# Kernel tuning notes

Measured on AMD Instinct MI355X. Metric: run time of the kernel, lower is better.

Reference implementation:

```python
import jax, jax.numpy as jnp
import numpy as np

B, N_N, N_A, D = 1024, 96, 96, 512


def _normalize(x):
    return x / jnp.linalg.norm(x, axis=-1, keepdims=True)


def setup_inputs() -> dict:
    key = jax.random.key(0)
    ks = jax.random.split(key, 8)
    img_embs = _normalize(jax.random.normal(ks[0], (B, D), jnp.float32))
    normal_text_embs = _normalize(jax.random.normal(ks[1], (N_N, D), jnp.float32))
    abnormal_text_embs = _normalize(jax.random.normal(ks[2], (N_A, D), jnp.float32))
    logit_scale = jnp.full((1,), np.log(100.0), jnp.float32)  # CLIP temperature
    W1 = jax.random.normal(ks[3], (2 * D, D), jnp.float32) / np.sqrt(2 * D)
    b1 = jnp.zeros((D,), jnp.float32)
    W2 = jax.random.normal(ks[4], (D, D // 2), jnp.float32) / np.sqrt(D)
    b2 = jnp.zeros((D // 2,), jnp.float32)
    W3 = jax.random.normal(ks[5], (D // 2, D // 4), jnp.float32) / np.sqrt(D // 2)
    b3 = jnp.zeros((D // 4,), jnp.float32)
    return {"img_embs": img_embs, "normal_text_embs": normal_text_embs,
            "abnormal_text_embs": abnormal_text_embs, "logit_scale": logit_scale,
            "W1": W1, "b1": b1, "W2": W2, "b2": b2, "W3": W3, "b3": b3}


def _mlp(x, W1, b1, W2, b2, W3, b3):
    h = jax.nn.relu(x @ W1 + b1)
    h = jax.nn.relu(h @ W2 + b2)
    return h @ W3 + b3


def _branch(img_embs, text_embs, scale, W1, b1, W2, b2, W3, b3):
    # sims: [B, N]; softmax weights then exp-scaled text embeddings
    sims = (img_embs @ text_embs.T) * scale
    w = jax.nn.softmax(sims, axis=-1)
    scaled_text = text_embs[None, :, :] * jnp.exp(w)[:, :, None]      # [B, N, D]
    rep_img = jnp.broadcast_to(img_embs[:, None, :], scaled_text.shape)  # [B, N, D]
    x = jnp.concatenate([rep_img, scaled_text], axis=-1)              # [B, N, 2D]
    h = _mlp(x, W1, b1, W2, b2, W3, b3)                               # [B, N, D//4]
    return h.mean(axis=1)                                             # [B, D//4]


def reference(img_embs, normal_text_embs, abnormal_text_embs, logit_scale,
              W1, b1, W2, b2, W3, b3):
    scale = jnp.exp(logit_scale[0])
    h_n = _branch(img_embs, normal_text_embs, scale, W1, b1, W2, b2, W3, b3)
    h_a = _branch(img_embs, abnormal_text_embs, scale, W1, b1, W2, b2, W3, b3)
    return (h_n, h_a)
```

## Files before the change

kernel.cpp:

```cpp
#include <hip/hip_runtime.h>
#include <hip/hip_bf16.h>


typedef __attribute__((ext_vector_type(8))) short short8;
typedef __attribute__((ext_vector_type(4))) float floatx4;
typedef __attribute__((ext_vector_type(4))) unsigned int uint4v;

__device__ __forceinline__ unsigned short f2bf(float x) {
    unsigned int u = __float_as_uint(x);
    u += 0x7fffu + ((u >> 16) & 1u);
    return (unsigned short)(u >> 16);
}
__device__ __forceinline__ float bf2f(unsigned short u) {
    return __uint_as_float(((unsigned int)u) << 16);
}

template <bool BF16OUT>
__device__ __forceinline__ void gemm64(
    const float* __restrict__ A0, const float* __restrict__ A1, int rows0,
    const float* __restrict__ Bm, float* __restrict__ Cf,
    unsigned short* __restrict__ Cb, int bx, int by,
    unsigned char* smem, int t) {
    float (*sAT)[68] = (float (*)[68])smem;
    int r0b = bx * 64, c0b = by * 64;
    int rg = t >> 4, cg = t & 15;
    int c0 = c0b + cg * 4;
    float acc[4][4];
#pragma unroll
    for (int r = 0; r < 4; r++)
#pragma unroll
        for (int c = 0; c < 4; c++) acc[r][c] = 0.f;

    for (int k0 = 0; k0 < 512; k0 += 32) {
#pragma unroll
        for (int i = 0; i < 2; i++) {
            int row = (t >> 3) + i * 32;
            int kk = (t & 7) * 4;
            int gr = r0b + row;
            const float* Ap = (gr < rows0) ? (A0 + gr * 512) : (A1 + (gr - rows0) * 512);
            float4 av = *(const float4*)(Ap + k0 + kk);
            sAT[kk + 0][row] = av.x; sAT[kk + 1][row] = av.y;
            sAT[kk + 2][row] = av.z; sAT[kk + 3][row] = av.w;
        }
        __syncthreads();
#pragma unroll
        for (int kk = 0; kk < 32; kk++) {
            float4 a = *(const float4*)(&sAT[kk][rg * 4]);
            float4 bv = *(const float4*)(Bm + (k0 + kk) * 512 + c0);
            float ar[4] = {a.x, a.y, a.z, a.w};
            float bc[4] = {bv.x, bv.y, bv.z, bv.w};
#pragma unroll
            for (int r = 0; r < 4; r++)
#pragma unroll
                for (int c = 0; c < 4; c++)
                    acc[r][c] = fmaf(ar[r], bc[c], acc[r][c]);
        }
        __syncthreads();
    }
    int r0 = r0b + rg * 4;
#pragma unroll
    for (int r = 0; r < 4; r++) {
        if (BF16OUT) {
            unsigned long long pk =
                (unsigned long long)f2bf(acc[r][0]) |
                ((unsigned long long)f2bf(acc[r][1]) << 16) |
                ((unsigned long long)f2bf(acc[r][2]) << 32) |
                ((unsigned long long)f2bf(acc[r][3]) << 48);
            *(unsigned long long*)(Cb + (r0 + r) * 512 + c0) = pk;
        } else {
            *(float4*)(Cf + (r0 + r) * 512 + c0) =
                make_float4(acc[r][0], acc[r][1], acc[r][2], acc[r][3]);
        }
    }
}

__global__ __launch_bounds__(256) void prep_kernel(
    const float* __restrict__ img, const float* __restrict__ tn,
    const float* __restrict__ ta, const float* __restrict__ ls,
    const float* __restrict__ W1, const float* __restrict__ W2,
    float* __restrict__ e_ws, float* __restrict__ U_ws,
    unsigned short* __restrict__ Tb, unsigned short* __restrict__ W2T) {
    __shared__ __align__(16) unsigned char smem[9216];
    int idx = blockIdx.x;
    int t = threadIdx.x;

    if (idx < 1024) {
        int b = idx;
        float* sImg = (float*)smem;
        float* sS   = sImg + 512;
        float* sMx  = sS + 192;
        float* sSum = sMx + 2;
        for (int i = t; i < 512; i += 256) sImg[i] = img[b * 512 + i];
        __syncthreads();
        float scale = __expf(ls[0]);
        int g = t & 7;
#pragma unroll
        for (int i = 0; i < 6; i++) {
            int n = (t >> 3) + 32 * i;
            const float* tx = (n < 96) ? (tn + n * 512) : (ta + (n - 96) * 512);
            float d = 0.f;
#pragma unroll
            for (int s = 0; s < 16; s++) {
                int k = g * 4 + s * 32;
                float4 x = *(const float4*)(tx + k);
                d += x.x * sImg[k] + x.y * sImg[k + 1] + x.z * sImg[k + 2] + x.w * sImg[k + 3];
            }
            d += __shfl_xor(d, 1);
            d += __shfl_xor(d, 2);
            d += __shfl_xor(d, 4);
            if (g == 0) sS[n] = d * scale;
        }
        __syncthreads();
        if (t < 2) {
            float m = -1e30f;
            for (int n = 0; n < 96; n++) m = fmaxf(m, sS[t * 96 + n]);
            float s = 0.f;
            for (int n = 0; n < 96; n++) s += __expf(sS[t * 96 + n] - m);
            sMx[t] = m; sSum[t] = s;
        }
        __syncthreads();
        if (t < 192) {
            int br = t / 96, n = t % 96;
            float w = __expf(sS[t] - sMx[br]) / sSum[br];
            e_ws[(br * 1024 + b) * 96 + n] = __expf(w);
        }
    } else if (idx < 1152) {
        int i = idx - 1024;
        gemm64<false>(img, img, 1 << 20, W1, U_ws, nullptr, i & 15, i >> 4, smem, t);
    } else if (idx < 1176) {
        int i = idx - 1152;
        gemm64<true>(tn, ta, 96, W1 + 512 * 512, nullptr, Tb, i % 3, i / 3, smem, t);
    } else {
        int i = idx - 1176;
        int n0 = i * 64;
        for (int r = 0; r < 64; r++) {
            int n = n0 + r;
            for (int k = t; k < 512; k += 256)
                W2T[n * 512 + k] = f2bf(W2[k * 256 + n]);
        }
    }
}

__global__ __launch_bounds__(256) void branch_mlp2(
    const float* __restrict__ U, const unsigned short* __restrict__ Tb,
    const float* __restrict__ e_all, const unsigned short* __restrict__ W2T,
    const float* __restrict__ b1, const float* __restrict__ b2,
    const float* __restrict__ W3, const float* __restrict__ b3,
    float* __restrict__ out) {
    int b = blockIdx.x, br = blockIdx.y;
    const unsigned short* T = Tb + br * (96 * 512);
    const float* e = e_all + (br * 1024 + b) * 96;

    __shared__ float sUb[512];
    __shared__ float sE[96];
    __shared__ __align__(16) unsigned short sH[96][88];
    __shared__ float sM2[256];
    __shared__ float sPart[256];

    int t = threadIdx.x;
    for (int i = t; i < 512; i += 256) sUb[i] = U[b * 512 + i] + b1[i];
    if (t < 96) sE[t] = e[t];
    __syncthreads();

    const int wave = t >> 6, lane = t & 63;
    const int frow = lane & 15, fkq = (lane >> 4) * 8;
    const int ncol0 = wave * 64;
    const int srow = t >> 3;
    const int skc = (t & 7) * 8;

    const floatx4 fz = {0.f, 0.f, 0.f, 0.f};
    floatx4 acc[6][4];
#pragma unroll
    for (int mt = 0; mt < 6; mt++)
#pragma unroll
        for (int j = 0; j < 4; j++) acc[mt][j] = fz;

    int trow[3]; float ev[3]; short8 tv[3];
#pragma unroll
    for (int i2 = 0; i2 < 3; i2++) {
        trow[i2] = srow + 32 * i2;
        ev[i2] = sE[trow[i2]];
        tv[i2] = *(const short8*)(T + trow[i2] * 512 + skc);
    }

#pragma unroll
    for (int kt = 0; kt < 8; kt++) {
        int k0 = kt * 64;
        float4 u0 = *(const float4*)(&sUb[k0 + skc]);
        float4 u1 = *(const float4*)(&sUb[k0 + skc + 4]);
        float ua[8] = {u0.x, u0.y, u0.z, u0.w, u1.x, u1.y, u1.z, u1.w};
#pragma unroll
        for (int i2 = 0; i2 < 3; i2++) {
            uint4v pk;
#pragma unroll
            for (int jj = 0; jj < 4; jj++) {
                float f0 = fmaxf(fmaf(ev[i2], bf2f((unsigned short)tv[i2][2 * jj]), ua[2 * jj]), 0.f);
                float f1 = fmaxf(fmaf(ev[i2], bf2f((unsigned short)tv[i2][2 * jj + 1]), ua[2 * jj + 1]), 0.f);
                __hip_bfloat162 h2 = __float22bfloat162_rn(make_float2(f0, f1));
                unsigned int bits;
                __builtin_memcpy(&bits, &h2, 4);
                pk[jj] = bits;
            }
            *(uint4v*)(&sH[trow[i2]][skc]) = pk;
        }
        __syncthreads();
        if (kt < 7) {
#pragma unroll
            for (int i2 = 0; i2 < 3; i2++)
                tv[i2] = *(const short8*)(T + trow[i2] * 512 + k0 + 64 + skc);
        }
#pragma unroll
        for (int ks = 0; ks < 2; ks++) {
            short8 bfr[4];
#pragma unroll
            for (int j = 0; j < 4; j++)
                bfr[j] = *(const short8*)(W2T + (ncol0 + j * 16 + frow) * 512 + k0 + ks * 32 + fkq);
#pragma unroll
            for (int mt = 0; mt < 6; mt++) {
                short8 afr = *(const short8*)(&sH[mt * 16 + frow][ks * 32 + fkq]);
#pragma unroll
                for (int j = 0; j < 4; j++)
                    acc[mt][j] = __builtin_amdgcn_mfma_f32_16x16x32_bf16(afr, bfr[j], acc[mt][j], 0, 0, 0);
            }
        }
        __syncthreads();
    }

#pragma unroll
    for (int j = 0; j < 4; j++) {
        int col = ncol0 + j * 16 + frow;
        float bb = b2[col];
        float s = 0.f;
#pragma unroll
        for (int mt = 0; mt < 6; mt++)
#pragma unroll
            for (int r = 0; r < 4; r++)
                s += fmaxf(acc[mt][j][r] + bb, 0.f);
        s += __shfl_xor(s, 16);
        s += __shfl_xor(s, 32);
        if (lane < 16) sM2[col] = s * (1.0f / 96.0f);
    }
    __syncthreads();

    int col = t & 127, ks2 = t >> 7;
    const float* w3p = W3 + (ks2 * 128) * 128 + col;
    const float* mp = sM2 + ks2 * 128;
    float o = 0.f;
#pragma unroll 8
    for (int k = 0; k < 128; k++) o = fmaf(mp[k], w3p[k * 128], o);
    sPart[t] = o;
    __syncthreads();
    if (t < 128) out[(br * 1024 + b) * 128 + t] = sPart[t] + sPart[t + 128] + b3[t];
}

extern "C" void kernel_launch(void* const* d_in, const int* in_sizes, int n_in,
                              void* d_out, int out_size, void* d_ws, size_t ws_size,
                              hipStream_t stream) {
    const float* img = (const float*)d_in[0];
    const float* tn  = (const float*)d_in[1];
    const float* ta  = (const float*)d_in[2];
    const float* ls  = (const float*)d_in[3];
    const float* W1  = (const float*)d_in[4];
    const float* b1  = (const float*)d_in[5];
    const float* W2  = (const float*)d_in[6];
    const float* b2  = (const float*)d_in[7];
    const float* W3  = (const float*)d_in[8];
    const float* b3  = (const float*)d_in[9];
    float* out = (float*)d_out;
    float* ws  = (float*)d_ws;

    float* e_ws = ws;
    float* U_ws = ws + 196608;
    unsigned short* Tb  = (unsigned short*)(ws + 720896);
    unsigned short* W2T = (unsigned short*)(ws + 770048);

    prep_kernel<<<1180, 256, 0, stream>>>(img, tn, ta, ls, W1, W2, e_ws, U_ws, Tb, W2T);
    branch_mlp2<<<dim3(1024, 2), 256, 0, stream>>>(U_ws, Tb, e_ws, W2T, b1, b2, W3, b3, out);
}
```

Before: 214.7 us.

## Build MFMA A-fragments in registers and use finer prep GEMM tiles

The branch MLP kernel no longer stages the relu'd layer-1 activations through shared memory with block barriers. Each wave now loads T rows straight from global memory in MFMA fragment layout and forms the bf16 A operand in registers. This removes the LDS round trip and the __syncthreads per k-tile. The cost is that every wave recomputes the same activation fragments (4x redundant elementwise work and T loads). Separately, the prep GEMMs switch from 64x64 register-blocked tiles to 16x64 tiles with one row per thread, giving many more blocks but less data reuse per block.

```diff
diff --git a/kernel.cpp b/kernel.cpp
--- a/kernel.cpp
+++ b/kernel.cpp
@@ -4,7 +4,6 @@
 
 typedef __attribute__((ext_vector_type(8))) short short8;
 typedef __attribute__((ext_vector_type(4))) float floatx4;
-typedef __attribute__((ext_vector_type(4))) unsigned int uint4v;
 
 __device__ __forceinline__ unsigned short f2bf(float x) {
     unsigned int u = __float_as_uint(x);
@@ -16,61 +15,38 @@
 }
 
 template <bool BF16OUT>
-__device__ __forceinline__ void gemm64(
+__device__ __forceinline__ void gemm16(
     const float* __restrict__ A0, const float* __restrict__ A1, int rows0,
     const float* __restrict__ Bm, float* __restrict__ Cf,
-    unsigned short* __restrict__ Cb, int bx, int by,
-    unsigned char* smem, int t) {
-    float (*sAT)[68] = (float (*)[68])smem;
-    int r0b = bx * 64, c0b = by * 64;
-    int rg = t >> 4, cg = t & 15;
-    int c0 = c0b + cg * 4;
-    float acc[4][4];
-#pragma unroll
-    for (int r = 0; r < 4; r++)
-#pragma unroll
-        for (int c = 0; c < 4; c++) acc[r][c] = 0.f;
-
+    unsigned short* __restrict__ Cb, int mt, int nt, float* sA , int t) {
+    int r0 = mt * 16, c0 = nt * 64;
+    int row = t >> 4, cg = t & 15;
+    int rglob = r0 + row;
+    const float* Ap = (rglob < rows0) ? (A0 + rglob * 512) : (A1 + (rglob - rows0) * 512);
+    float a0 = 0.f, a1 = 0.f, a2 = 0.f, a3 = 0.f;
+    const float* Bp = Bm + c0 + cg * 4;
     for (int k0 = 0; k0 < 512; k0 += 32) {
-#pragma unroll
-        for (int i = 0; i < 2; i++) {
-            int row = (t >> 3) + i * 32;
-            int kk = (t & 7) * 4;
-            int gr = r0b + row;
-            const float* Ap = (gr < rows0) ? (A0 + gr * 512) : (A1 + (gr - rows0) * 512);
-            float4 av = *(const float4*)(Ap + k0 + kk);
-            sAT[kk + 0][row] = av.x; sAT[kk + 1][row] = av.y;
-            sAT[kk + 2][row] = av.z; sAT[kk + 3][row] = av.w;
-        }
-        __syncthreads();
-#pragma unroll
+        __syncthreads();
+        float2 av = *(const float2*)(Ap + k0 + cg * 2);
+        sA[row * 33 + cg * 2] = av.x;
+        sA[row * 33 + cg * 2 + 1] = av.y;
+        __syncthreads();
+#pragma unroll 8
         for (int kk = 0; kk < 32; kk++) {
-            float4 a = *(const float4*)(&sAT[kk][rg * 4]);
-            float4 bv = *(const float4*)(Bm + (k0 + kk) * 512 + c0);
-            float ar[4] = {a.x, a.y, a.z, a.w};
-            float bc[4] = {bv.x, bv.y, bv.z, bv.w};
-#pragma unroll
-            for (int r = 0; r < 4; r++)
-#pragma unroll
-                for (int c = 0; c < 4; c++)
-                    acc[r][c] = fmaf(ar[r], bc[c], acc[r][c]);
-        }
-        __syncthreads();
-    }
-    int r0 = r0b + rg * 4;
-#pragma unroll
-    for (int r = 0; r < 4; r++) {
-        if (BF16OUT) {
-            unsigned long long pk =
-                (unsigned long long)f2bf(acc[r][0]) |
-                ((unsigned long long)f2bf(acc[r][1]) << 16) |
-                ((unsigned long long)f2bf(acc[r][2]) << 32) |
-                ((unsigned long long)f2bf(acc[r][3]) << 48);
-            *(unsigned long long*)(Cb + (r0 + r) * 512 + c0) = pk;
-        } else {
-            *(float4*)(Cf + (r0 + r) * 512 + c0) =
-                make_float4(acc[r][0], acc[r][1], acc[r][2], acc[r][3]);
-        }
+            float a = sA[row * 33 + kk];
+            float4 bv = *(const float4*)(Bp + (k0 + kk) * 512);
+            a0 = fmaf(a, bv.x, a0); a1 = fmaf(a, bv.y, a1);
+            a2 = fmaf(a, bv.z, a2); a3 = fmaf(a, bv.w, a3);
+        }
+    }
+    int c = c0 + cg * 4;
+    if (BF16OUT) {
+        unsigned long long pk =
+            (unsigned long long)f2bf(a0) | ((unsigned long long)f2bf(a1) << 16) |
+            ((unsigned long long)f2bf(a2) << 32) | ((unsigned long long)f2bf(a3) << 48);
+        *(unsigned long long*)(Cb + rglob * 512 + c) = pk;
+    } else {
+        *(float4*)(Cf + rglob * 512 + c) = make_float4(a0, a1, a2, a3);
     }
 }
 
@@ -80,16 +56,16 @@
     const float* __restrict__ W1, const float* __restrict__ W2,
     float* __restrict__ e_ws, float* __restrict__ U_ws,
     unsigned short* __restrict__ Tb, unsigned short* __restrict__ W2T) {
-    __shared__ __align__(16) unsigned char smem[9216];
+    __shared__ __align__(16) float smem[720];
     int idx = blockIdx.x;
     int t = threadIdx.x;
 
     if (idx < 1024) {
         int b = idx;
-        float* sImg = (float*)smem;
-        float* sS   = sImg + 512;
-        float* sMx  = sS + 192;
-        float* sSum = sMx + 2;
+        float* sImg = smem;
+        float* sS   = smem + 512;
+        float* sMx  = smem + 704;
+        float* sSum = smem + 706;
         for (int i = t; i < 512; i += 256) sImg[i] = img[b * 512 + i];
         __syncthreads();
         float scale = __expf(ls[0]);
@@ -124,24 +100,23 @@
             float w = __expf(sS[t] - sMx[br]) / sSum[br];
             e_ws[(br * 1024 + b) * 96 + n] = __expf(w);
         }
-    } else if (idx < 1152) {
+    } else if (idx < 1536) {
         int i = idx - 1024;
-        gemm64<false>(img, img, 1 << 20, W1, U_ws, nullptr, i & 15, i >> 4, smem, t);
-    } else if (idx < 1176) {
-        int i = idx - 1152;
-        gemm64<true>(tn, ta, 96, W1 + 512 * 512, nullptr, Tb, i % 3, i / 3, smem, t);
+        gemm16<false>(img, img, 1 << 20, W1, U_ws, nullptr, i >> 3, i & 7, smem, t);
+    } else if (idx < 1632) {
+        int i = idx - 1536;
+        gemm16<true>(tn, ta, 96, W1 + 512 * 512, nullptr, Tb, i >> 3, i & 7, smem, t);
     } else {
-        int i = idx - 1176;
-        int n0 = i * 64;
-        for (int r = 0; r < 64; r++) {
-            int n = n0 + r;
+        int i = idx - 1632;
+        for (int r = 0; r < 16; r++) {
+            int n = i * 16 + r;
             for (int k = t; k < 512; k += 256)
                 W2T[n * 512 + k] = f2bf(W2[k * 256 + n]);
         }
     }
 }
 
-__global__ __launch_bounds__(256) void branch_mlp2(
+__global__ __launch_bounds__(256) void branch_mlp3(
     const float* __restrict__ U, const unsigned short* __restrict__ Tb,
     const float* __restrict__ e_all, const unsigned short* __restrict__ W2T,
     const float* __restrict__ b1, const float* __restrict__ b2,
@@ -149,24 +124,24 @@
     float* __restrict__ out) {
     int b = blockIdx.x, br = blockIdx.y;
     const unsigned short* T = Tb + br * (96 * 512);
-    const float* e = e_all + (br * 1024 + b) * 96;
 
     __shared__ float sUb[512];
     __shared__ float sE[96];
-    __shared__ __align__(16) unsigned short sH[96][88];
     __shared__ float sM2[256];
     __shared__ float sPart[256];
 
     int t = threadIdx.x;
     for (int i = t; i < 512; i += 256) sUb[i] = U[b * 512 + i] + b1[i];
-    if (t < 96) sE[t] = e[t];
+    if (t < 96) sE[t] = e_all[(br * 1024 + b) * 96 + t];
     __syncthreads();
 
     const int wave = t >> 6, lane = t & 63;
     const int frow = lane & 15, fkq = (lane >> 4) * 8;
     const int ncol0 = wave * 64;
-    const int srow = t >> 3;
-    const int skc = (t & 7) * 8;
+
+    float ev[6];
+#pragma unroll
+    for (int mt = 0; mt < 6; mt++) ev[mt] = sE[mt * 16 + frow];
 
     const floatx4 fz = {0.f, 0.f, 0.f, 0.f};
     floatx4 acc[6][4];
@@ -175,55 +150,36 @@
 #pragma unroll
         for (int j = 0; j < 4; j++) acc[mt][j] = fz;
 
-    int trow[3]; float ev[3]; short8 tv[3];
-#pragma unroll
-    for (int i2 = 0; i2 < 3; i2++) {
-        trow[i2] = srow + 32 * i2;
-        ev[i2] = sE[trow[i2]];
-        tv[i2] = *(const short8*)(T + trow[i2] * 512 + skc);
-    }
-
-#pragma unroll
-    for (int kt = 0; kt < 8; kt++) {
-        int k0 = kt * 64;
-        float4 u0 = *(const float4*)(&sUb[k0 + skc]);
-        float4 u1 = *(const float4*)(&sUb[k0 + skc + 4]);
+    const unsigned short* Trow = T + frow * 512 + fkq;
+    const unsigned short* Brow = W2T + (ncol0 + frow) * 512 + fkq;
+
+#pragma unroll 2
+    for (int s = 0; s < 16; s++) {
+        int k0 = s * 32;
+        float4 u0 = *(const float4*)(&sUb[k0 + fkq]);
+        float4 u1 = *(const float4*)(&sUb[k0 + fkq + 4]);
         float ua[8] = {u0.x, u0.y, u0.z, u0.w, u1.x, u1.y, u1.z, u1.w};
-#pragma unroll
-        for (int i2 = 0; i2 < 3; i2++) {
-            uint4v pk;
+        short8 bfr[4];
+#pragma unroll
+        for (int j = 0; j < 4; j++)
+            bfr[j] = *(const short8*)(Brow + j * (16 * 512) + k0);
+#pragma unroll
+        for (int mt = 0; mt < 6; mt++) {
+            short8 tv = *(const short8*)(Trow + mt * (16 * 512) + k0);
+            short8 afr;
 #pragma unroll
             for (int jj = 0; jj < 4; jj++) {
-                float f0 = fmaxf(fmaf(ev[i2], bf2f((unsigned short)tv[i2][2 * jj]), ua[2 * jj]), 0.f);
-                float f1 = fmaxf(fmaf(ev[i2], bf2f((unsigned short)tv[i2][2 * jj + 1]), ua[2 * jj + 1]), 0.f);
+                float f0 = fmaxf(fmaf(ev[mt], bf2f((unsigned short)tv[2 * jj]), ua[2 * jj]), 0.f);
+                float f1 = fmaxf(fmaf(ev[mt], bf2f((unsigned short)tv[2 * jj + 1]), ua[2 * jj + 1]), 0.f);
                 __hip_bfloat162 h2 = __float22bfloat162_rn(make_float2(f0, f1));
                 unsigned int bits;
                 __builtin_memcpy(&bits, &h2, 4);
-                pk[jj] = bits;
+                ((unsigned int*)&afr)[jj] = bits;
             }
-            *(uint4v*)(&sH[trow[i2]][skc]) = pk;
-        }
-        __syncthreads();
-        if (kt < 7) {
-#pragma unroll
-            for (int i2 = 0; i2 < 3; i2++)
-                tv[i2] = *(const short8*)(T + trow[i2] * 512 + k0 + 64 + skc);
-        }
-#pragma unroll
-        for (int ks = 0; ks < 2; ks++) {
-            short8 bfr[4];
 #pragma unroll
             for (int j = 0; j < 4; j++)
-                bfr[j] = *(const short8*)(W2T + (ncol0 + j * 16 + frow) * 512 + k0 + ks * 32 + fkq);
-#pragma unroll
-            for (int mt = 0; mt < 6; mt++) {
-                short8 afr = *(const short8*)(&sH[mt * 16 + frow][ks * 32 + fkq]);
-#pragma unroll
-                for (int j = 0; j < 4; j++)
-                    acc[mt][j] = __builtin_amdgcn_mfma_f32_16x16x32_bf16(afr, bfr[j], acc[mt][j], 0, 0, 0);
-            }
-        }
-        __syncthreads();
+                acc[mt][j] = __builtin_amdgcn_mfma_f32_16x16x32_bf16(afr, bfr[j], acc[mt][j], 0, 0, 0);
+        }
     }
 
 #pragma unroll
@@ -274,6 +230,6 @@
     unsigned short* Tb  = (unsigned short*)(ws + 720896);
     unsigned short* W2T = (unsigned short*)(ws + 770048);
 
-    prep_kernel<<<1180, 256, 0, stream>>>(img, tn, ta, ls, W1, W2, e_ws, U_ws, Tb, W2T);
-    branch_mlp2<<<dim3(1024, 2), 256, 0, stream>>>(U_ws, Tb, e_ws, W2T, b1, b2, W3, b3, out);
-}
+    prep_kernel<<<1648, 256, 0, stream>>>(img, tn, ta, ls, W1, W2, e_ws, U_ws, Tb, W2T);
+    branch_mlp3<<<dim3(1024, 2), 256, 0, stream>>>(U_ws, Tb, e_ws, W2T, b1, b2, W3, b3, out);
+}
```

New measurement: 325.3 us. 1.52x slower.

## Double-buffer hidden tile in LDS and prefetch W2 fragments across k-steps

Applied to the files above, without the earlier changes.

The hidden-activation LDS tile becomes double-buffered, which removes the second barrier per k-iteration. W2T fragments for the next k-step are prefetched into registers before the barrier so global load latency overlaps with compute. Launch bounds now request two blocks per CU. The trade-off is extra register and LDS pressure, and the tighter launch bound could force register spills.

```diff
diff --git a/kernel.cpp b/kernel.cpp
--- a/kernel.cpp
+++ b/kernel.cpp
@@ -141,7 +141,7 @@
     }
 }
 
-__global__ __launch_bounds__(256) void branch_mlp2(
+__global__ __launch_bounds__(256, 2) void branch_mlp4(
     const float* __restrict__ U, const unsigned short* __restrict__ Tb,
     const float* __restrict__ e_all, const unsigned short* __restrict__ W2T,
     const float* __restrict__ b1, const float* __restrict__ b2,
@@ -149,17 +149,16 @@
     float* __restrict__ out) {
     int b = blockIdx.x, br = blockIdx.y;
     const unsigned short* T = Tb + br * (96 * 512);
-    const float* e = e_all + (br * 1024 + b) * 96;
 
     __shared__ float sUb[512];
     __shared__ float sE[96];
-    __shared__ __align__(16) unsigned short sH[96][88];
+    __shared__ __align__(16) unsigned short sH[2][96][88];
     __shared__ float sM2[256];
     __shared__ float sPart[256];
 
     int t = threadIdx.x;
     for (int i = t; i < 512; i += 256) sUb[i] = U[b * 512 + i] + b1[i];
-    if (t < 96) sE[t] = e[t];
+    if (t < 96) sE[t] = e_all[(br * 1024 + b) * 96 + t];
     __syncthreads();
 
     const int wave = t >> 6, lane = t & 63;
@@ -182,10 +181,15 @@
         ev[i2] = sE[trow[i2]];
         tv[i2] = *(const short8*)(T + trow[i2] * 512 + skc);
     }
-
-#pragma unroll
-    for (int kt = 0; kt < 8; kt++) {
-        int k0 = kt * 64;
+    const unsigned short* Bbase = W2T + (ncol0 + frow) * 512 + fkq;
+    short8 bpre[4];
+#pragma unroll
+    for (int j = 0; j < 4; j++)
+        bpre[j] = *(const short8*)(Bbase + j * (16 * 512));
+
+#pragma unroll
+    for (int s = 0; s < 8; s++) {
+        int k0 = s * 64;
         float4 u0 = *(const float4*)(&sUb[k0 + skc]);
         float4 u1 = *(const float4*)(&sUb[k0 + skc + 4]);
         float ua[8] = {u0.x, u0.y, u0.z, u0.w, u1.x, u1.y, u1.z, u1.w};
@@ -201,29 +205,38 @@
                 __builtin_memcpy(&bits, &h2, 4);
                 pk[jj] = bits;
             }
-            *(uint4v*)(&sH[trow[i2]][skc]) = pk;
-        }
-        __syncthreads();
-        if (kt < 7) {
+            *(uint4v*)(&sH[s & 1][trow[i2]][skc]) = pk;
+        }
+        short8 bcur0[4];
+#pragma unroll
+        for (int j = 0; j < 4; j++) bcur0[j] = bpre[j];
+        if (s < 7) {
 #pragma unroll
             for (int i2 = 0; i2 < 3; i2++)
                 tv[i2] = *(const short8*)(T + trow[i2] * 512 + k0 + 64 + skc);
-        }
-#pragma unroll
-        for (int ks = 0; ks < 2; ks++) {
-            short8 bfr[4];
 #pragma unroll
             for (int j = 0; j < 4; j++)
-                bfr[j] = *(const short8*)(W2T + (ncol0 + j * 16 + frow) * 512 + k0 + ks * 32 + fkq);
-#pragma unroll
-            for (int mt = 0; mt < 6; mt++) {
-                short8 afr = *(const short8*)(&sH[mt * 16 + frow][ks * 32 + fkq]);
-#pragma unroll
-                for (int j = 0; j < 4; j++)
-                    acc[mt][j] = __builtin_amdgcn_mfma_f32_16x16x32_bf16(afr, bfr[j], acc[mt][j], 0, 0, 0);
-            }
-        }
-        __syncthreads();
+                bpre[j] = *(const short8*)(Bbase + j * (16 * 512) + k0 + 64);
+        }
+        __syncthreads();
+        short8 b1f[4];
+#pragma unroll
+        for (int j = 0; j < 4; j++)
+            b1f[j] = *(const short8*)(Bbase + j * (16 * 512) + k0 + 32);
+#pragma unroll
+        for (int mt = 0; mt < 6; mt++) {
+            short8 afr = *(const short8*)(&sH[s & 1][mt * 16 + frow][fkq]);
+#pragma unroll
+            for (int j = 0; j < 4; j++)
+                acc[mt][j] = __builtin_amdgcn_mfma_f32_16x16x32_bf16(afr, bcur0[j], acc[mt][j], 0, 0, 0);
+        }
+#pragma unroll
+        for (int mt = 0; mt < 6; mt++) {
+            short8 afr = *(const short8*)(&sH[s & 1][mt * 16 + frow][32 + fkq]);
+#pragma unroll
+            for (int j = 0; j < 4; j++)
+                acc[mt][j] = __builtin_amdgcn_mfma_f32_16x16x32_bf16(afr, b1f[j], acc[mt][j], 0, 0, 0);
+        }
     }
 
 #pragma unroll
@@ -275,5 +288,5 @@
     unsigned short* W2T = (unsigned short*)(ws + 770048);
 
     prep_kernel<<<1180, 256, 0, stream>>>(img, tn, ta, ls, W1, W2, e_ws, U_ws, Tb, W2T);
-    branch_mlp2<<<dim3(1024, 2), 256, 0, stream>>>(U_ws, Tb, e_ws, W2T, b1, b2, W3, b3, out);
-}
+    branch_mlp4<<<dim3(1024, 2), 256, 0, stream>>>(U_ws, Tb, e_ws, W2T, b1, b2, W3, b3, out);
+}
```

New measurement: 206.0 us. 1.04x faster.
